# Performance work log

Hardware: AMD Instinct MI355X
Metric: run time of the kernel (lower is better)

The kernel has to match this reference:

```python
import jax, jax.numpy as jnp
import numpy as np

N = 50000      # num_nodes
E = 800000     # undirected edge count (maps holds 2E directed maps)
D = 4          # stalk dimension


def setup_inputs() -> dict:
    key = jax.random.key(0)
    k1, k2, k3 = jax.random.split(key, 3)
    maps = jax.random.normal(k1, (2 * E, D, D), dtype=jnp.float32) * 0.3
    # ensure every node appears as a source at least once (avoids degenerate
    # identity eigenproblems for isolated nodes)
    row = jnp.concatenate([jnp.arange(N, dtype=jnp.int32),
                           jax.random.randint(k2, (E - N,), 0, N, dtype=jnp.int32)])
    col = jax.random.randint(k3, (E,), 0, N, dtype=jnp.int32)
    # second half of edge_index is the reversed orientation, as the module assumes
    edge_index = jnp.stack([jnp.concatenate([row, col]),
                            jnp.concatenate([col, row])])
    return {"maps": maps, "edge_index": edge_index, "num_nodes": N}


def reference(maps, edge_index, num_nodes):
    n = num_nodes
    d = maps.shape[1]
    twoE = maps.shape[0]
    Ee = twoE // 2
    row_all = edge_index[0]                                   # [2E]
    # diag contribution: R^T R per directed edge, scatter-added onto source node
    diag_contrib = jnp.einsum('eki,ekj->eij', maps, maps)     # [2E,d,d]
    maps_diag = jnp.zeros((n, d, d), maps.dtype).at[row_all].add(diag_contrib)
    row = edge_index[0, :Ee]
    col = edge_index[1, :Ee]
    # off-diagonal block: R_ij^T R_ji per undirected edge
    maps_triu = jnp.einsum('eki,ekj->eij', maps[:Ee], maps[Ee:])  # [E,d,d]
    # eval-mode augmentation: + I
    to_inv = maps_diag + jnp.eye(d, dtype=maps.dtype)
    evals, evecs = jnp.linalg.eigh(to_inv)                    # batched tiny eigh
    inv_sqrt = jnp.einsum('nik,nk,njk->nij', evecs,
                          jnp.clip(evals, 1e-8, None) ** -0.5, evecs)
    # normalize: D^{-1/2} blocks, clamp to [-1, 1]
    maps_triu = jnp.clip(jnp.einsum('eik,ekl,elj->eij',
                                    inv_sqrt[row], maps_triu, inv_sqrt[col]), -1.0, 1.0)
    maps_diag = jnp.clip(jnp.einsum('nik,nkl,nlj->nij',
                                    inv_sqrt, maps_diag, inv_sqrt), -1.0, 1.0)
    # COO assembly of the (n*d, n*d) sheaf Laplacian
    ar = jnp.arange(d, dtype=jnp.int32)
    A, B = jnp.meshgrid(ar, ar, indexing='ij')                # [d,d]
    node = jnp.arange(n, dtype=jnp.int32)
    diag_rows = (node[:, None, None] * d + A).reshape(-1)
    diag_cols = (node[:, None, None] * d + B).reshape(-1)
    tri_rows_ij = (row[:, None, None] * d + A).reshape(-1)
    tri_cols_ij = (col[:, None, None] * d + B).reshape(-1)
    tri_rows_ji = (col[:, None, None] * d + A).reshape(-1)
    tri_cols_ji = (row[:, None, None] * d + B).reshape(-1)
    rows = jnp.concatenate([diag_rows, tri_rows_ij, tri_rows_ji])
    cols = jnp.concatenate([diag_cols, tri_cols_ij, tri_cols_ji])
    vals = jnp.concatenate([maps_diag.reshape(-1),
                            (-maps_triu).reshape(-1),
                            (-jnp.swapaxes(maps_triu, 1, 2)).reshape(-1)])
    indices = jnp.stack([rows, cols])                         # [2, K]
    return indices, vals
```

## Files before the change

### kernel.cpp

```cpp
#include <hip/hip_runtime.h>

#define DEG_CAP 96

__device__ __forceinline__ void load4x4(const float* __restrict__ p, float m[4][4]) {
    const float4* q = (const float4*)p;
#pragma unroll
    for (int k = 0; k < 4; ++k) {
        float4 v = q[k];
        m[k][0] = v.x; m[k][1] = v.y; m[k][2] = v.z; m[k][3] = v.w;
    }
}

__device__ __forceinline__ void store4x4(float* __restrict__ p, const float m[4][4]) {
    float4* q = (float4*)p;
#pragma unroll
    for (int k = 0; k < 4; ++k)
        q[k] = make_float4(m[k][0], m[k][1], m[k][2], m[k][3]);
}

__device__ __forceinline__ void mmTa(const float a[4][4], const float b[4][4], float o[4][4]) {
#pragma unroll
    for (int i = 0; i < 4; ++i)
#pragma unroll
        for (int j = 0; j < 4; ++j)
            o[i][j] = a[0][i]*b[0][j] + a[1][i]*b[1][j] + a[2][i]*b[2][j] + a[3][i]*b[3][j];
}

__device__ __forceinline__ void mm(const float a[4][4], const float b[4][4], float o[4][4]) {
#pragma unroll
    for (int i = 0; i < 4; ++i)
#pragma unroll
        for (int j = 0; j < 4; ++j)
            o[i][j] = a[i][0]*b[0][j] + a[i][1]*b[1][j] + a[i][2]*b[2][j] + a[i][3]*b[3][j];
}

__global__ void k_fill(const int* __restrict__ ei, int* __restrict__ cnt,
                       int* __restrict__ bucket, int twoE, int N) {
    int e = blockIdx.x * blockDim.x + threadIdx.x;
    if (e >= twoE) return;
    int node = ei[e];
    int slot = atomicAdd(&cnt[(size_t)node * 16], 1);
    if (slot < DEG_CAP)
        bucket[(size_t)slot * N + node] = e;
}

__global__ void k_gather(const float* __restrict__ maps, const int* __restrict__ cnt,
                         const int* __restrict__ bucket, float* __restrict__ Rtab,
                         float* __restrict__ out_vals, int N) {
    int n = blockIdx.x * blockDim.x + threadIdx.x;
    if (n >= N) return;
    int d = cnt[(size_t)n * 16];
    if (d > DEG_CAP) d = DEG_CAP;
    float G[10];
#pragma unroll
    for (int t = 0; t < 10; ++t) G[t] = 0.0f;
    for (int k = 0; k < d; ++k) {
        int e = bucket[(size_t)k * N + n];
        float m[4][4];
        load4x4(maps + (size_t)e * 16, m);
        int t = 0;
#pragma unroll
        for (int i = 0; i < 4; ++i)
#pragma unroll
            for (int j = i; j < 4; ++j, ++t)
                G[t] += m[0][i]*m[0][j] + m[1][i]*m[1][j] + m[2][i]*m[2][j] + m[3][i]*m[3][j];
    }
    float D[4][4];
    {
        int t = 0;
#pragma unroll
        for (int i = 0; i < 4; ++i)
#pragma unroll
            for (int j = i; j < 4; ++j, ++t) { D[i][j] = G[t]; D[j][i] = G[t]; }
    }
    float A[4][4], V[4][4];
#pragma unroll
    for (int i = 0; i < 4; ++i)
#pragma unroll
        for (int j = 0; j < 4; ++j) {
            A[i][j] = D[i][j] + (i == j ? 1.0f : 0.0f);
            V[i][j] = (i == j) ? 1.0f : 0.0f;
        }
    const int PP[6] = {0,0,0,1,1,2};
    const int QQ[6] = {1,2,3,2,3,3};
    for (int sweep = 0; sweep < 6; ++sweep) {
        for (int r = 0; r < 6; ++r) {
            int p = PP[r], q = QQ[r];
            float apq = A[p][q];
            if (fabsf(apq) < 1e-12f) continue;
            float tau = (A[q][q] - A[p][p]) / (2.0f * apq);
            float t = copysignf(1.0f, tau) / (fabsf(tau) + sqrtf(1.0f + tau * tau));
            float c = 1.0f / sqrtf(1.0f + t * t);
            float s = t * c;
#pragma unroll
            for (int k = 0; k < 4; ++k) {
                float akp = A[k][p], akq = A[k][q];
                A[k][p] = c * akp - s * akq;
                A[k][q] = s * akp + c * akq;
            }
#pragma unroll
            for (int k = 0; k < 4; ++k) {
                float apk = A[p][k], aqk = A[q][k];
                A[p][k] = c * apk - s * aqk;
                A[q][k] = s * apk + c * aqk;
            }
#pragma unroll
            for (int k = 0; k < 4; ++k) {
                float vkp = V[k][p], vkq = V[k][q];
                V[k][p] = c * vkp - s * vkq;
                V[k][q] = s * vkp + c * vkq;
            }
        }
    }
    float w[4];
#pragma unroll
    for (int k = 0; k < 4; ++k)
        w[k] = 1.0f / sqrtf(fmaxf(A[k][k], 1e-8f));
    float R[4][4];
#pragma unroll
    for (int i = 0; i < 4; ++i)
#pragma unroll
        for (int j = 0; j < 4; ++j)
            R[i][j] = V[i][0]*w[0]*V[j][0] + V[i][1]*w[1]*V[j][1]
                    + V[i][2]*w[2]*V[j][2] + V[i][3]*w[3]*V[j][3];
    store4x4(Rtab + (size_t)n * 16, R);
    float U[4][4], O[4][4];
    mm(R, D, U);
    mm(U, R, O);
#pragma unroll
    for (int i = 0; i < 4; ++i)
#pragma unroll
        for (int j = 0; j < 4; ++j)
            O[i][j] = fminf(fmaxf(O[i][j], -1.0f), 1.0f);
    store4x4(out_vals + (size_t)n * 16, O);
}

__global__ void k_edge(const float* __restrict__ maps, const int* __restrict__ ei,
                       const float* __restrict__ Rtab,
                       float* __restrict__ out, size_t Tot, int N, int E) {
    int e = blockIdx.x * blockDim.x + threadIdx.x;
    if (e >= E) return;
    float M1[4][4], M2[4][4];
    load4x4(maps + (size_t)e * 16, M1);
    load4x4(maps + (size_t)(E + e) * 16, M2);
    int r = ei[e];
    int c = ei[2 * E + e];
    float T[4][4];
    mmTa(M1, M2, T);
    float Rr[4][4], Rc[4][4];
    load4x4(Rtab + (size_t)r * 16, Rr);
    load4x4(Rtab + (size_t)c * 16, Rc);
    float U[4][4], S[4][4];
    mm(Rr, T, U);
    mm(U, Rc, S);
#pragma unroll
    for (int i = 0; i < 4; ++i)
#pragma unroll
        for (int j = 0; j < 4; ++j)
            S[i][j] = fminf(fmaxf(S[i][j], -1.0f), 1.0f);

    float* out_rows = out;
    float* out_cols = out + Tot;
    float* out_vals = out + 2 * Tot;

    float rb = (float)(r * 4);
    float cb = (float)(c * 4);

    {
        size_t base = (size_t)16 * N + (size_t)e * 16;
        float4* qr = (float4*)(out_rows + base);
        float4* qc = (float4*)(out_cols + base);
        float4* qv = (float4*)(out_vals + base);
#pragma unroll
        for (int i = 0; i < 4; ++i) {
            float ri = rb + (float)i;
            qr[i] = make_float4(ri, ri, ri, ri);
            qc[i] = make_float4(cb, cb + 1.0f, cb + 2.0f, cb + 3.0f);
            qv[i] = make_float4(-S[i][0], -S[i][1], -S[i][2], -S[i][3]);
        }
    }
    {
        size_t base = (size_t)16 * (N + (size_t)E) + (size_t)e * 16;
        float4* qr = (float4*)(out_rows + base);
        float4* qc = (float4*)(out_cols + base);
        float4* qv = (float4*)(out_vals + base);
#pragma unroll
        for (int i = 0; i < 4; ++i) {
            float ci = cb + (float)i;
            qr[i] = make_float4(ci, ci, ci, ci);
            qc[i] = make_float4(rb, rb + 1.0f, rb + 2.0f, rb + 3.0f);
            qv[i] = make_float4(-S[0][i], -S[1][i], -S[2][i], -S[3][i]);
        }
    }
}

__global__ void k_nodeB(float* __restrict__ out, size_t Tot, int N) {
    int n = blockIdx.x * blockDim.x + threadIdx.x;
    if (n >= N) return;
    float nb = (float)(n * 4);
    float4* qr = (float4*)(out + (size_t)n * 16);
    float4* qc = (float4*)(out + Tot + (size_t)n * 16);
#pragma unroll
    for (int i = 0; i < 4; ++i) {
        float ni = nb + (float)i;
        qr[i] = make_float4(ni, ni, ni, ni);
        qc[i] = make_float4(nb, nb + 1.0f, nb + 2.0f, nb + 3.0f);
    }
}

extern "C" void kernel_launch(void* const* d_in, const int* in_sizes, int n_in,
                              void* d_out, int out_size, void* d_ws, size_t ws_size,
                              hipStream_t stream) {
    const float* maps = (const float*)d_in[0];
    const int* ei = (const int*)d_in[1];

    int twoE = in_sizes[0] / 16;
    int E = twoE / 2;
    size_t Tot = (size_t)out_size / 3;
    int N = (int)(Tot / 16) - twoE;

    float* out = (float*)d_out;
    float* out_vals = out + 2 * Tot;

    int* bucket = (int*)(out + ((size_t)out_size - (size_t)DEG_CAP * N));
    int* cnt    = (int*)(out + ((size_t)out_size - (size_t)DEG_CAP * N - (size_t)N * 16));
    float* Rtab = out;

    hipMemsetAsync(cnt, 0, (size_t)N * 16 * sizeof(int), stream);

    int bs = 256;
    k_fill<<<(twoE + bs - 1) / bs, bs, 0, stream>>>(ei, cnt, bucket, twoE, N);
    k_gather<<<(N + bs - 1) / bs, bs, 0, stream>>>(maps, cnt, bucket, Rtab, out_vals, N);
    k_edge<<<(E + bs - 1) / bs, bs, 0, stream>>>(maps, ei, Rtab, out, Tot, N, E);
    k_nodeB<<<(N + bs - 1) / bs, bs, 0, stream>>>(out, Tot, N);
}
```

Baseline: 638.2 us.

## Replace bucket-gather diag accumulation with per-edge float atomic scatter

```diff
diff --git a/kernel.cpp b/kernel.cpp
--- a/kernel.cpp
+++ b/kernel.cpp
@@ -1,6 +1,4 @@
 #include <hip/hip_runtime.h>
-
-#define DEG_CAP 96
 
 __device__ __forceinline__ void load4x4(const float* __restrict__ p, float m[4][4]) {
     const float4* q = (const float4*)p;
@@ -34,37 +32,42 @@
             o[i][j] = a[i][0]*b[0][j] + a[i][1]*b[1][j] + a[i][2]*b[2][j] + a[i][3]*b[3][j];
 }
 
-__global__ void k_fill(const int* __restrict__ ei, int* __restrict__ cnt,
-                       int* __restrict__ bucket, int twoE, int N) {
+__global__ void k_scatter(const float* __restrict__ maps, const int* __restrict__ ei,
+                          float* __restrict__ gram, int E) {
     int e = blockIdx.x * blockDim.x + threadIdx.x;
-    if (e >= twoE) return;
-    int node = ei[e];
-    int slot = atomicAdd(&cnt[(size_t)node * 16], 1);
-    if (slot < DEG_CAP)
-        bucket[(size_t)slot * N + node] = e;
-}
-
-__global__ void k_gather(const float* __restrict__ maps, const int* __restrict__ cnt,
-                         const int* __restrict__ bucket, float* __restrict__ Rtab,
-                         float* __restrict__ out_vals, int N) {
+    if (e >= E) return;
+    float M1[4][4], M2[4][4];
+    load4x4(maps + (size_t)e * 16, M1);
+    load4x4(maps + (size_t)(E + e) * 16, M2);
+    int r = ei[e];
+    int c = ei[E + e];
+    float Ga[10], Gb[10];
+    {
+        int t = 0;
+#pragma unroll
+        for (int i = 0; i < 4; ++i)
+#pragma unroll
+            for (int j = i; j < 4; ++j, ++t) {
+                Ga[t] = M1[0][i]*M1[0][j] + M1[1][i]*M1[1][j] + M1[2][i]*M1[2][j] + M1[3][i]*M1[3][j];
+                Gb[t] = M2[0][i]*M2[0][j] + M2[1][i]*M2[1][j] + M2[2][i]*M2[2][j] + M2[3][i]*M2[3][j];
+            }
+    }
+    float* gr = gram + (size_t)r * 16;
+    float* gc = gram + (size_t)c * 16;
+#pragma unroll
+    for (int t = 0; t < 10; ++t) atomicAdd(&gr[t], Ga[t]);
+#pragma unroll
+    for (int t = 0; t < 10; ++t) atomicAdd(&gc[t], Gb[t]);
+}
+
+__global__ void k_diag(const float* __restrict__ gram, float* __restrict__ Rtab,
+                       float* __restrict__ out_vals, int N) {
     int n = blockIdx.x * blockDim.x + threadIdx.x;
     if (n >= N) return;
-    int d = cnt[(size_t)n * 16];
-    if (d > DEG_CAP) d = DEG_CAP;
+    const float* g = gram + (size_t)n * 16;
     float G[10];
 #pragma unroll
-    for (int t = 0; t < 10; ++t) G[t] = 0.0f;
-    for (int k = 0; k < d; ++k) {
-        int e = bucket[(size_t)k * N + n];
-        float m[4][4];
-        load4x4(maps + (size_t)e * 16, m);
-        int t = 0;
-#pragma unroll
-        for (int i = 0; i < 4; ++i)
-#pragma unroll
-            for (int j = i; j < 4; ++j, ++t)
-                G[t] += m[0][i]*m[0][j] + m[1][i]*m[1][j] + m[2][i]*m[2][j] + m[3][i]*m[3][j];
-    }
+    for (int t = 0; t < 10; ++t) G[t] = g[t];
     float D[4][4];
     {
         int t = 0;
@@ -222,15 +225,14 @@
     float* out = (float*)d_out;
     float* out_vals = out + 2 * Tot;
 
-    int* bucket = (int*)(out + ((size_t)out_size - (size_t)DEG_CAP * N));
-    int* cnt    = (int*)(out + ((size_t)out_size - (size_t)DEG_CAP * N - (size_t)N * 16));
+    float* gram = out + ((size_t)out_size - (size_t)N * 16);
     float* Rtab = out;
 
-    hipMemsetAsync(cnt, 0, (size_t)N * 16 * sizeof(int), stream);
+    hipMemsetAsync(gram, 0, (size_t)N * 16 * sizeof(float), stream);
 
     int bs = 256;
-    k_fill<<<(twoE + bs - 1) / bs, bs, 0, stream>>>(ei, cnt, bucket, twoE, N);
-    k_gather<<<(N + bs - 1) / bs, bs, 0, stream>>>(maps, cnt, bucket, Rtab, out_vals, N);
+    k_scatter<<<(E + bs - 1) / bs, bs, 0, stream>>>(maps, ei, gram, E);
+    k_diag<<<(N + bs - 1) / bs, bs, 0, stream>>>(gram, Rtab, out_vals, N);
     k_edge<<<(E + bs - 1) / bs, bs, 0, stream>>>(maps, ei, Rtab, out, Tot, N, E);
     k_nodeB<<<(N + bs - 1) / bs, bs, 0, stream>>>(out, Tot, N);
 }
```

Result: slower. 1.272 ms (+99.4%).

## Split node gather into wave-per-node Gram reduction plus separate eigen kernel

Applied to the files above, without the earlier changes.

```diff
diff --git a/kernel.cpp b/kernel.cpp
--- a/kernel.cpp
+++ b/kernel.cpp
@@ -44,27 +44,57 @@
         bucket[(size_t)slot * N + node] = e;
 }
 
-__global__ void k_gather(const float* __restrict__ maps, const int* __restrict__ cnt,
-                         const int* __restrict__ bucket, float* __restrict__ Rtab,
-                         float* __restrict__ out_vals, int N) {
-    int n = blockIdx.x * blockDim.x + threadIdx.x;
+__global__ void k_gather_wave(const float* __restrict__ maps, const int* __restrict__ cnt,
+                              const int* __restrict__ bucket, float* __restrict__ gram,
+                              int N) {
+    int tid = blockIdx.x * blockDim.x + threadIdx.x;
+    int n = tid >> 6;
+    int lane = threadIdx.x & 63;
     if (n >= N) return;
     int d = cnt[(size_t)n * 16];
     if (d > DEG_CAP) d = DEG_CAP;
+
     float G[10];
 #pragma unroll
     for (int t = 0; t < 10; ++t) G[t] = 0.0f;
-    for (int k = 0; k < d; ++k) {
-        int e = bucket[(size_t)k * N + n];
-        float m[4][4];
-        load4x4(maps + (size_t)e * 16, m);
-        int t = 0;
-#pragma unroll
-        for (int i = 0; i < 4; ++i)
-#pragma unroll
-            for (int j = i; j < 4; ++j, ++t)
-                G[t] += m[0][i]*m[0][j] + m[1][i]*m[1][j] + m[2][i]*m[2][j] + m[3][i]*m[3][j];
-    }
+
+#pragma unroll
+    for (int rep = 0; rep < 2; ++rep) {
+        int slot = lane + rep * 64;
+        if (slot < d) {
+            int e = bucket[(size_t)slot * N + n];
+            float m[4][4];
+            load4x4(maps + (size_t)e * 16, m);
+            int t = 0;
+#pragma unroll
+            for (int i = 0; i < 4; ++i)
+#pragma unroll
+                for (int j = i; j < 4; ++j, ++t)
+                    G[t] += m[0][i]*m[0][j] + m[1][i]*m[1][j] + m[2][i]*m[2][j] + m[3][i]*m[3][j];
+        }
+    }
+#pragma unroll
+    for (int msk = 1; msk < 64; msk <<= 1) {
+#pragma unroll
+        for (int t = 0; t < 10; ++t)
+            G[t] += __shfl_xor(G[t], msk, 64);
+    }
+    if (lane == 0) {
+        float* g = gram + (size_t)n * 16;
+        *(float4*)(g)     = make_float4(G[0], G[1], G[2], G[3]);
+        *(float4*)(g + 4) = make_float4(G[4], G[5], G[6], G[7]);
+        *(float2*)(g + 8) = make_float2(G[8], G[9]);
+    }
+}
+
+__global__ void k_diag(const float* __restrict__ gram, float* __restrict__ Rtab,
+                       float* __restrict__ out_vals, int N) {
+    int n = blockIdx.x * blockDim.x + threadIdx.x;
+    if (n >= N) return;
+    const float* g = gram + (size_t)n * 16;
+    float G[10];
+#pragma unroll
+    for (int t = 0; t < 10; ++t) G[t] = g[t];
     float D[4][4];
     {
         int t = 0;
@@ -224,13 +254,15 @@
 
     int* bucket = (int*)(out + ((size_t)out_size - (size_t)DEG_CAP * N));
     int* cnt    = (int*)(out + ((size_t)out_size - (size_t)DEG_CAP * N - (size_t)N * 16));
+    float* gram =        out + ((size_t)out_size - (size_t)DEG_CAP * N - (size_t)N * 32);
     float* Rtab = out;
 
     hipMemsetAsync(cnt, 0, (size_t)N * 16 * sizeof(int), stream);
 
     int bs = 256;
     k_fill<<<(twoE + bs - 1) / bs, bs, 0, stream>>>(ei, cnt, bucket, twoE, N);
-    k_gather<<<(N + bs - 1) / bs, bs, 0, stream>>>(maps, cnt, bucket, Rtab, out_vals, N);
+    k_gather_wave<<<((size_t)N * 64 + bs - 1) / bs, bs, 0, stream>>>(maps, cnt, bucket, gram, N);
+    k_diag<<<(N + bs - 1) / bs, bs, 0, stream>>>(gram, Rtab, out_vals, N);
     k_edge<<<(E + bs - 1) / bs, bs, 0, stream>>>(maps, ei, Rtab, out, Tot, N, E);
     k_nodeB<<<(N + bs - 1) / bs, bs, 0, stream>>>(out, Tot, N);
 }
```

Result: no change. 628.2 us (-1.6%).
